# Optimization experiments

Hardware: AMD Instinct MI355X
Metric: run time of the kernel (lower is better)

Reference implementation:

```python
import jax, jax.numpy as jnp
import numpy as np

B, N, K = 4, 4096, 16
D_POINTS, D_MODEL = 64, 128


def setup_inputs() -> dict:
    key = jax.random.key(0)
    ks = jax.random.split(key, 18)
    rn = lambda k, shp, s=0.05: (jax.random.normal(k, shp, jnp.float32) * s)
    return {
        "xyz": jax.random.normal(ks[0], (B, N, 3), jnp.float32),
        "features": jax.random.normal(ks[1], (B, N, D_POINTS), jnp.float32),
        # fc_delta: Linear(3,d_model) -> ReLU -> Linear(d_model,d_model)
        "Wd1": rn(ks[2], (3, D_MODEL)), "bd1": rn(ks[3], (D_MODEL,)),
        "Wd2": rn(ks[4], (D_MODEL, D_MODEL)), "bd2": rn(ks[5], (D_MODEL,)),
        # fc1: Linear(d_points, d_model)
        "Wf1": rn(ks[6], (D_POINTS, D_MODEL)), "bf1": rn(ks[7], (D_MODEL,)),
        # w_qs / w_ks / w_vs: Linear(d_model, d_model, bias=False)
        "Wq": rn(ks[8], (D_MODEL, D_MODEL)),
        "Wk": rn(ks[9], (D_MODEL, D_MODEL)),
        "Wv": rn(ks[10], (D_MODEL, D_MODEL)),
        # fc_gamma: Linear(d_model,d_model) -> ReLU -> Linear(d_model,d_model)
        "Wg1": rn(ks[11], (D_MODEL, D_MODEL)), "bg1": rn(ks[12], (D_MODEL,)),
        "Wg2": rn(ks[13], (D_MODEL, D_MODEL)), "bg2": rn(ks[14], (D_MODEL,)),
        # fc2: Linear(d_model, d_points)
        "Wo": rn(ks[15], (D_MODEL, D_POINTS)), "bo": rn(ks[16], (D_POINTS,)),
    }


def reference(xyz, features, Wd1, bd1, Wd2, bd2, Wf1, bf1, Wq, Wk, Wv,
              Wg1, bg1, Wg2, bg2, Wo, bo):
    sq = jnp.sum(xyz * xyz, axis=-1)
    d2 = sq[:, :, None] + sq[:, None, :] - 2.0 * jnp.einsum('bnd,bmd->bnm', xyz, xyz)
    # argsort()[:, :, :k] == k smallest distances (self included)
    _, knn_idx = jax.lax.top_k(-d2, K)  # [B,N,K] int32

    gather = jax.vmap(lambda a, i: a[i])  # per-batch fancy gather along point axis
    knn_xyz = gather(xyz, knn_idx)                       # [B,N,K,3]
    rel = xyz[:, :, None, :] - knn_xyz                   # [B,N,K,3]
    pos_enc = jax.nn.relu(rel @ Wd1 + bd1) @ Wd2 + bd2   # [B,N,K,D]

    shortcut = features
    f = features @ Wf1 + bf1                             # [B,N,D]
    knn_f = gather(f, knn_idx)                           # [B,N,K,D]

    q = f @ Wq                                           # [B,N,D]
    k = knn_f @ Wk                                       # [B,N,K,D]
    v = knn_f @ Wv                                       # [B,N,K,D]

    attn = q[:, :, None, :] - k + pos_enc                # [B,N,K,D]
    attn = jax.nn.relu(attn @ Wg1 + bg1) @ Wg2 + bg2
    attn = jax.nn.softmax(attn / np.sqrt(D_MODEL).astype(np.float32), axis=-2)

    res = jnp.einsum('bnkf,bnkf->bnf', attn, v + pos_enc)  # [B,N,D]
    return res @ Wo + bo + shortcut                        # [B,N,d_points]
```

## Files before the change

### kernel.cpp

```cpp
#include <hip/hip_runtime.h>
#include <hip/hip_bf16.h>

#define NPTS 4096
#define BATCH 4
#define BN (BATCH * NPTS)
#define DMODEL 128
#define DPTS 64
#define KNBR 16
#define SWS 136

typedef unsigned short u16;
typedef unsigned int u32;
typedef unsigned long long u64;
typedef short bh8 __attribute__((ext_vector_type(8)));
typedef float f32x4 __attribute__((ext_vector_type(4)));

__device__ __forceinline__ float bfu(u16 u) {
    union { u32 i; float f; } c; c.i = ((u32)u) << 16; return c.f;
}
__device__ __forceinline__ u16 f2u(float x) {
    u32 u = __float_as_uint(x);
    u32 r = u + 0x7FFFu + ((u >> 16) & 1u);
    return (u16)(r >> 16);
}
__device__ __forceinline__ u32 pack2(float a, float b) {
    return (u32)f2u(a) | ((u32)f2u(b) << 16);
}
__device__ __forceinline__ float ldr(const void* p, long i, int mode) {
    return mode == 0 ? bfu(((const u16*)p)[i]) : ((const float*)p)[i];
}
__device__ __forceinline__ void str(void* p, long i, float v, int mode) {
    if (mode == 0) ((u16*)p)[i] = f2u(v);
    else ((float*)p)[i] = v;
}
__device__ __forceinline__ int detect_mode(const void* Wq) {
    const u16* w = (const u16*)Wq;
    int lane = threadIdx.x & 63;
    int tot = 0;
#pragma unroll
    for (int r = 0; r < 4; ++r) {
        unsigned e = (w[lane + r * 64] >> 7) & 0xFFu;
        bool wild = (e >= 132u) || (e > 0u && e <= 90u);
        tot += (int)__popcll(__ballot(wild));
    }
    return tot > 32 ? 1 : 0;
}

__global__ __launch_bounds__(256) void prep_kernel(
    const void* __restrict__ Wd2, const void* __restrict__ Wg1, const void* __restrict__ Wg2,
    const void* __restrict__ Wo, const void* __restrict__ Wq, const void* __restrict__ Wk,
    const void* __restrict__ Wv, const void* __restrict__ Wf1, const void* __restrict__ xyz,
    u16* __restrict__ WdT2, u16* __restrict__ WgT1, u16* __restrict__ WgT2,
    u16* __restrict__ WoT, u16* __restrict__ WqT, u16* __restrict__ WkT,
    u16* __restrict__ WvT, u16* __restrict__ WfT, uint2* __restrict__ cloud) {
    int mode = detect_mode(Wq);
    int gid = blockIdx.x * 256 + threadIdx.x;
    if (gid < 6 * 16384) {
        int m = gid >> 14, o = gid & 16383;
        int n = o >> 7, i = o & 127;
        const void* W = (m == 0) ? Wd2 : (m == 1) ? Wg1 : (m == 2) ? Wg2
                      : (m == 3) ? Wq  : (m == 4) ? Wk  : Wv;
        u16* D = (m == 0) ? WdT2 : (m == 1) ? WgT1 : (m == 2) ? WgT2
               : (m == 3) ? WqT  : (m == 4) ? WkT  : WvT;
        D[o] = f2u(ldr(W, (long)i * 128 + n, mode));
    } else if (gid < 6 * 16384 + 8192) {
        int o = gid - 6 * 16384;
        int n = o >> 6, k2 = o & 63;
        WfT[o] = f2u(ldr(Wf1, (long)k2 * 128 + n, mode));
    } else if (gid < 6 * 16384 + 16384) {
        int o2 = gid - 6 * 16384 - 8192;
        int col = o2 >> 7, i = o2 & 127;
        WoT[o2] = f2u(ldr(Wo, (long)i * 64 + col, mode));
    } else if (gid < 6 * 16384 + 16384 + 16384) {
        int i = gid - (6 * 16384 + 16384);
        float gx = ldr(xyz, (long)i * 3 + 0, mode);
        float gy = ldr(xyz, (long)i * 3 + 1, mode);
        float gz = ldr(xyz, (long)i * 3 + 2, mode);
        uint2 pk;
        pk.x = (u32)f2u(gx) | ((u32)f2u(gy) << 16);
        pk.y = (u32)f2u(gz);
        cloud[i] = pk;
    }
}

__global__ __launch_bounds__(256) void qkv_kernel(
    const void* __restrict__ feat, const void* __restrict__ bf1v, const void* __restrict__ WqRaw,
    const u16* __restrict__ WfT, const u16* __restrict__ WqT,
    const u16* __restrict__ WkT, const u16* __restrict__ WvT,
    u16* __restrict__ qw, u16* __restrict__ kfw, u16* __restrict__ vfw) {
    int mode = detect_mode(WqRaw);
    __shared__ __align__(16) u16 sFeat[64 * 72];
    __shared__ __align__(16) u16 sF[64 * SWS];
    const int t = threadIdx.x;
    const int p0 = blockIdx.x * 64;
    const int lane = t & 63, w = t >> 6;
    const int rg = (w & 1) * 32, cg = (w >> 1) * 64;
    const int lm = lane & 15, lq = lane >> 4;

    for (int i = t; i < 512; i += 256) {
        int r = i >> 3, c8 = i & 7;
        u16 tmp[8];
        if (mode == 0) {
            *(uint4*)tmp = *((const uint4*)feat + (long)(p0 + r) * 8 + c8);
        } else {
            const float* fp = (const float*)feat + (long)(p0 + r) * 64 + c8 * 8;
#pragma unroll
            for (int u = 0; u < 8; ++u) tmp[u] = f2u(fp[u]);
        }
        *(uint4*)(sFeat + r * 72 + c8 * 8) = *(uint4*)tmp;
    }
    __syncthreads();

    {
        f32x4 acc[2][4];
#pragma unroll
        for (int rt = 0; rt < 2; ++rt)
#pragma unroll
            for (int ct = 0; ct < 4; ++ct) { acc[rt][ct][0]=0.f; acc[rt][ct][1]=0.f; acc[rt][ct][2]=0.f; acc[rt][ct][3]=0.f; }
#pragma unroll
        for (int kk = 0; kk < 2; ++kk) {
            const int ko = kk * 32 + lq * 8;
            bh8 a0 = *(const bh8*)(sFeat + (rg + lm) * 72 + ko);
            bh8 a1 = *(const bh8*)(sFeat + (rg + 16 + lm) * 72 + ko);
            bh8 bq[4];
#pragma unroll
            for (int ct = 0; ct < 4; ++ct)
                bq[ct] = *(const bh8*)(WfT + (long)(cg + ct * 16 + lm) * 64 + ko);
#pragma unroll
            for (int ct = 0; ct < 4; ++ct) {
                acc[0][ct] = __builtin_amdgcn_mfma_f32_16x16x32_bf16(a0, bq[ct], acc[0][ct], 0, 0, 0);
                acc[1][ct] = __builtin_amdgcn_mfma_f32_16x16x32_bf16(a1, bq[ct], acc[1][ct], 0, 0, 0);
            }
        }
#pragma unroll
        for (int rt = 0; rt < 2; ++rt)
#pragma unroll
            for (int ct = 0; ct < 4; ++ct) {
                const int col = cg + ct * 16 + lm;
                const float bj = ldr(bf1v, col, mode);
#pragma unroll
                for (int r4 = 0; r4 < 4; ++r4) {
                    int row = rg + rt * 16 + lq * 4 + r4;
                    u32 u = (u32)f2u(acc[rt][ct][r4] + bj);
                    u32 o = __shfl_xor(u, 1);
                    if ((lane & 1) == 0)
                        *(u32*)(sF + row * SWS + col) = u | (o << 16);
                }
            }
    }
    __syncthreads();

    {
        const int m = blockIdx.y;
        const u16* Wm = (m == 0) ? WqT : (m == 1) ? WkT : WvT;
        u16* Om = (m == 0) ? qw : (m == 1) ? kfw : vfw;
        f32x4 acc[2][4];
#pragma unroll
        for (int rt = 0; rt < 2; ++rt)
#pragma unroll
            for (int ct = 0; ct < 4; ++ct) { acc[rt][ct][0]=0.f; acc[rt][ct][1]=0.f; acc[rt][ct][2]=0.f; acc[rt][ct][3]=0.f; }
#pragma unroll
        for (int kk = 0; kk < 4; ++kk) {
            const int ko = kk * 32 + lq * 8;
            bh8 a0 = *(const bh8*)(sF + (rg + lm) * SWS + ko);
            bh8 a1 = *(const bh8*)(sF + (rg + 16 + lm) * SWS + ko);
            bh8 bq[4];
#pragma unroll
            for (int ct = 0; ct < 4; ++ct)
                bq[ct] = *(const bh8*)(Wm + (long)(cg + ct * 16 + lm) * 128 + ko);
#pragma unroll
            for (int ct = 0; ct < 4; ++ct) {
                acc[0][ct] = __builtin_amdgcn_mfma_f32_16x16x32_bf16(a0, bq[ct], acc[0][ct], 0, 0, 0);
                acc[1][ct] = __builtin_amdgcn_mfma_f32_16x16x32_bf16(a1, bq[ct], acc[1][ct], 0, 0, 0);
            }
        }
#pragma unroll
        for (int rt = 0; rt < 2; ++rt)
#pragma unroll
            for (int ct = 0; ct < 4; ++ct) {
                const int col = cg + ct * 16 + lm;
#pragma unroll
                for (int r4 = 0; r4 < 4; ++r4) {
                    int row = rg + rt * 16 + lq * 4 + r4;
                    u32 u = (u32)f2u(acc[rt][ct][r4]);
                    u32 o = __shfl_xor(u, 1);
                    if ((lane & 1) == 0)
                        *(u32*)(Om + (long)(p0 + row) * DMODEL + col) = u | (o << 16);
                }
            }
    }
}

__global__ __launch_bounds__(256) void knn_kernel(
    const uint2* __restrict__ cloud, int* __restrict__ knnIdx) {
    const int t = threadIdx.x, lane = t & 63, w = t >> 6;
    const int p0 = blockIdx.x * 4;
    const long bbase = (long)(p0 >> 12) * NPTS;
    const uint2* cl = cloud + bbase;

    const int pl = (p0 & (NPTS - 1)) + w;
    uint2 qv = cl[pl];
    const float px = __uint_as_float(qv.x << 16);
    const float py = __uint_as_float(qv.x & 0xFFFF0000u);
    const float pz = __uint_as_float(qv.y << 16);

    u64 kv;
    {
        uint2 c = cl[lane];
        float cx = __uint_as_float(c.x << 16);
        float cy = __uint_as_float(c.x & 0xFFFF0000u);
        float cz = __uint_as_float(c.y << 16);
        float key = fmaf(px * cx + py * cy + pz * cz, -2.f,
                         cx * cx + cy * cy + cz * cz);
        u32 uk = __float_as_uint(key);
        uk ^= (u32)((int)uk >> 31) | 0x80000000u;
        kv = ((u64)uk << 32) | (u32)lane;
#pragma unroll
        for (int k = 2; k <= 64; k <<= 1) {
#pragma unroll
            for (int j = k >> 1; j > 0; j >>= 1) {
                u64 other = __shfl_xor(kv, j);
                bool keepMin = ((lane & j) == 0) == ((lane & k) == 0);
                bool smaller = kv < other;
                kv = (keepMin == smaller) ? kv : other;
            }
        }
    }
    u32 Tu = __builtin_amdgcn_readlane((u32)(kv >> 32), 15);

    uint2 cd0 = cl[64 + lane];
    uint2 cd1 = cl[128 + lane];
#pragma unroll 1
    for (int it = 0; it < 32; ++it) {
        const int base = 64 + it * 128;
        uint2 c0 = cd0, c1 = cd1;
        if (it < 31) {
            int n0 = base + 128 + lane;
            int n1 = n0 + 64 > 4095 ? 4095 : n0 + 64;
            cd0 = cl[n0];
            cd1 = cl[n1];
        }
        float cx0 = __uint_as_float(c0.x << 16);
        float cy0 = __uint_as_float(c0.x & 0xFFFF0000u);
        float cz0 = __uint_as_float(c0.y << 16);
        float cx1 = __uint_as_float(c1.x << 16);
        float cy1 = __uint_as_float(c1.x & 0xFFFF0000u);
        float cz1 = __uint_as_float(c1.y << 16);
        float k0 = fmaf(px * cx0 + py * cy0 + pz * cz0, -2.f,
                        cx0 * cx0 + cy0 * cy0 + cz0 * cz0);
        float k1 = fmaf(px * cx1 + py * cy1 + pz * cz1, -2.f,
                        cx1 * cx1 + cy1 * cy1 + cz1 * cz1);
        u32 u0 = __float_as_uint(k0); u0 ^= (u32)((int)u0 >> 31) | 0x80000000u;
        u32 u1 = __float_as_uint(k1); u1 ^= (u32)((int)u1 >> 31) | 0x80000000u;
        if (it == 31) u1 = 0xFFFFFFFFu;
        u32 umin = (u0 < u1) ? u0 : u1;
        unsigned long long mask = __ballot(umin < Tu);
        while (mask) {
            int l = __ffsll(mask) - 1;
            mask &= mask - 1;
            u32 a0 = __builtin_amdgcn_readlane(u0, l);
            u32 a1 = __builtin_amdgcn_readlane(u1, l);
            if (a0 < Tu) {
                u64 cand = ((u64)a0 << 32) | (u32)(base + l);
                u64 prev = __shfl_up(kv, 1);
                if (lane == 0) prev = 0;
                kv = (prev > cand) ? prev : ((kv > cand) ? cand : kv);
                Tu = __builtin_amdgcn_readlane((u32)(kv >> 32), 15);
            }
            if (a1 < Tu) {
                u64 cand = ((u64)a1 << 32) | (u32)(base + 64 + l);
                u64 prev = __shfl_up(kv, 1);
                if (lane == 0) prev = 0;
                kv = (prev > cand) ? prev : ((kv > cand) ? cand : kv);
                Tu = __builtin_amdgcn_readlane((u32)(kv >> 32), 15);
            }
        }
    }
    if (lane < 16) knnIdx[(long)(p0 + w) * 16 + lane] = (int)(u32)kv;
}

#define ATT_SA 0
#define ATT_SPE 17408
#define ATT_SREL 34816
#define ATT_SBIAS 35840
#define ATT_SQ 37376
#define SMEM_BYTES 38400

__global__ __launch_bounds__(256, 4) void fused_kernel(
    const uint2* __restrict__ cloud, const int* __restrict__ knnIdx,
    const void* __restrict__ feat,
    const void* __restrict__ Wd1, const void* __restrict__ bd1, const void* __restrict__ bd2,
    const void* __restrict__ bg1, const void* __restrict__ bg2, const void* __restrict__ bo,
    const void* __restrict__ WqRaw,
    const u16* __restrict__ WdT2, const u16* __restrict__ WgT1, const u16* __restrict__ WgT2,
    const u16* __restrict__ WoT,
    const u16* __restrict__ qw, const u16* __restrict__ kfw, const u16* __restrict__ vfw,
    void* __restrict__ out) {
    int mode = detect_mode(WqRaw);
    __shared__ __align__(16) char smem[SMEM_BYTES];
    __shared__ int sIdx[64];
    u16* sA   = (u16*)(smem + ATT_SA);
    u16* sPE  = (u16*)(smem + ATT_SPE);
    float (*sRel)[4] = (float(*)[4])(smem + ATT_SREL);
    float* sBias = (float*)(smem + ATT_SBIAS);
    u16* sQ   = (u16*)(smem + ATT_SQ);

    const int t = threadIdx.x, lane = t & 63, w = t >> 6;
    const int lm = lane & 15, lq = lane >> 4;
    const int p0 = blockIdx.x * 4;
    const long bbase = (long)(p0 >> 12) * NPTS;
    const uint2* cl = cloud + bbase;

    for (int i = t; i < 384; i += 256) {
        const void* b = (i < 128) ? bd2 : (i < 256) ? bg1 : bg2;
        sBias[i] = ldr(b, i & 127, mode);
    }
    ((u32*)sQ)[t] = ((const u32*)(qw + (long)p0 * DMODEL))[t];
    const int ch = 2 * lane;
    const float wd0a = ldr(Wd1, ch, mode),       wd0b = ldr(Wd1, ch + 1, mode);
    const float wd1a = ldr(Wd1, 128 + ch, mode), wd1b = ldr(Wd1, 128 + ch + 1, mode);
    const float wd2a = ldr(Wd1, 256 + ch, mode), wd2b = ldr(Wd1, 256 + ch + 1, mode);
    const float bd1a = ldr(bd1, ch, mode),       bd1b = ldr(bd1, ch + 1, mode);
    if (t < 64) {
        int idx = knnIdx[(long)p0 * 16 + t];
        sIdx[t] = idx;
        int pl2 = (p0 & (NPTS - 1)) + (t >> 4);
        uint2 pv = cl[pl2];
        uint2 nv = cl[idx];
        sRel[t][0] = __uint_as_float(pv.x << 16)          - __uint_as_float(nv.x << 16);
        sRel[t][1] = __uint_as_float(pv.x & 0xFFFF0000u)  - __uint_as_float(nv.x & 0xFFFF0000u);
        sRel[t][2] = __uint_as_float(pv.y << 16)          - __uint_as_float(nv.y << 16);
    }
    __syncthreads();

#pragma unroll
    for (int i = 0; i < 16; ++i) {
        int r = w * 16 + i;
        float4 rl = *(const float4*)sRel[r];
        float h0 = fmaxf(bd1a + rl.x * wd0a + rl.y * wd1a + rl.z * wd2a, 0.f);
        float h1 = fmaxf(bd1b + rl.x * wd0b + rl.y * wd1b + rl.z * wd2b, 0.f);
        *(u32*)(sA + r * SWS + ch) = pack2(h0, h1);
    }
    __syncthreads();
    {
        const int rg = (w & 1) * 32, cg = (w >> 1) * 64;
        f32x4 acc[2][4];
#pragma unroll
        for (int rt = 0; rt < 2; ++rt)
#pragma unroll
            for (int ct = 0; ct < 4; ++ct) { acc[rt][ct][0]=0.f; acc[rt][ct][1]=0.f; acc[rt][ct][2]=0.f; acc[rt][ct][3]=0.f; }
#pragma unroll
        for (int kk = 0; kk < 4; ++kk) {
            const int ko = kk * 32 + lq * 8;
            bh8 a0 = *(const bh8*)(sA + (rg + lm) * SWS + ko);
            bh8 a1 = *(const bh8*)(sA + (rg + 16 + lm) * SWS + ko);
            bh8 bq[4];
#pragma unroll
            for (int ct = 0; ct < 4; ++ct)
                bq[ct] = *(const bh8*)(WdT2 + (long)(cg + ct * 16 + lm) * 128 + ko);
#pragma unroll
            for (int ct = 0; ct < 4; ++ct) {
                acc[0][ct] = __builtin_amdgcn_mfma_f32_16x16x32_bf16(a0, bq[ct], acc[0][ct], 0, 0, 0);
                acc[1][ct] = __builtin_amdgcn_mfma_f32_16x16x32_bf16(a1, bq[ct], acc[1][ct], 0, 0, 0);
            }
        }
#pragma unroll
        for (int rt = 0; rt < 2; ++rt)
#pragma unroll
            for (int ct = 0; ct < 4; ++ct) {
                const int col = cg + ct * 16 + lm;
                const float bj = sBias[col];
#pragma unroll
                for (int r4 = 0; r4 < 4; ++r4) {
                    int row = rg + rt * 16 + lq * 4 + r4;
                    u32 u = (u32)f2u(acc[rt][ct][r4] + bj);
                    u32 o = __shfl_xor(u, 1);
                    if ((lane & 1) == 0)
                        *(u32*)(sPE + row * SWS + col) = u | (o << 16);
                }
            }
    }
    __syncthreads();

#pragma unroll
    for (int i = 0; i < 16; ++i) {
        int r = w * 16 + i;
        u32 kv2 = *(const u32*)(kfw + (bbase + sIdx[r]) * (long)DMODEL + ch);
        u32 qv2 = *(const u32*)(sQ + (r >> 4) * DMODEL + ch);
        u32 pe2 = *(const u32*)(sPE + r * SWS + ch);
        float a0 = bfu((u16)qv2) - bfu((u16)kv2) + bfu((u16)pe2);
        float a1 = bfu((u16)(qv2 >> 16)) - bfu((u16)(kv2 >> 16)) + bfu((u16)(pe2 >> 16));
        *(u32*)(sA + r * SWS + ch) = pack2(a0, a1);
    }
    __syncthreads();
#pragma unroll 1
    for (int g = 0; g < 2; ++g) {
        const u16* Bg = (g == 0) ? WgT1 : WgT2;
        const float* bias = sBias + 128 + g * 128;
        const bool dorelu = (g == 0);
        const int rg = (w & 1) * 32, cg = (w >> 1) * 64;
        f32x4 acc[2][4];
#pragma unroll
        for (int rt = 0; rt < 2; ++rt)
#pragma unroll
            for (int ct = 0; ct < 4; ++ct) { acc[rt][ct][0]=0.f; acc[rt][ct][1]=0.f; acc[rt][ct][2]=0.f; acc[rt][ct][3]=0.f; }
#pragma unroll
        for (int kk = 0; kk < 4; ++kk) {
            const int ko = kk * 32 + lq * 8;
            bh8 a0 = *(const bh8*)(sA + (rg + lm) * SWS + ko);
            bh8 a1 = *(const bh8*)(sA + (rg + 16 + lm) * SWS + ko);
            bh8 bq[4];
#pragma unroll
            for (int ct = 0; ct < 4; ++ct)
                bq[ct] = *(const bh8*)(Bg + (long)(cg + ct * 16 + lm) * 128 + ko);
#pragma unroll
            for (int ct = 0; ct < 4; ++ct) {
                acc[0][ct] = __builtin_amdgcn_mfma_f32_16x16x32_bf16(a0, bq[ct], acc[0][ct], 0, 0, 0);
                acc[1][ct] = __builtin_amdgcn_mfma_f32_16x16x32_bf16(a1, bq[ct], acc[1][ct], 0, 0, 0);
            }
        }
        __syncthreads();
#pragma unroll
        for (int rt = 0; rt < 2; ++rt)
#pragma unroll
            for (int ct = 0; ct < 4; ++ct) {
                const int col = cg + ct * 16 + lm;
                const float bj = bias[col];
#pragma unroll
                for (int r4 = 0; r4 < 4; ++r4) {
                    int row = rg + rt * 16 + lq * 4 + r4;
                    float v = acc[rt][ct][r4] + bj;
                    if (dorelu) v = fmaxf(v, 0.f);
                    u32 u = (u32)f2u(v);
                    u32 o = __shfl_xor(u, 1);
                    if ((lane & 1) == 0)
                        *(u32*)(sA + row * SWS + col) = u | (o << 16);
                }
            }
        __syncthreads();
    }

    float res0, res1;
    {
        float mx0 = -3e38f, mx1 = -3e38f;
#pragma unroll
        for (int k = 0; k < KNBR; ++k) {
            u32 l2 = *(const u32*)(sA + (w * 16 + k) * SWS + ch);
            mx0 = fmaxf(mx0, bfu((u16)l2));
            mx1 = fmaxf(mx1, bfu((u16)(l2 >> 16)));
        }
        const float inv = 0.08838834764831845f;
        float s0 = 0.f, s1 = 0.f, r0 = 0.f, r1 = 0.f;
#pragma unroll
        for (int k = 0; k < KNBR; ++k) {
            u32 l2 = *(const u32*)(sA + (w * 16 + k) * SWS + ch);
            u32 v2 = *(const u32*)(vfw + (bbase + sIdx[w * 16 + k]) * (long)DMODEL + ch);
            u32 p2 = *(const u32*)(sPE + (w * 16 + k) * SWS + ch);
            float e0 = __expf((bfu((u16)l2) - mx0) * inv);
            float e1 = __expf((bfu((u16)(l2 >> 16)) - mx1) * inv);
            s0 += e0; s1 += e1;
            r0 += e0 * (bfu((u16)v2) + bfu((u16)p2));
            r1 += e1 * (bfu((u16)(v2 >> 16)) + bfu((u16)(p2 >> 16)));
        }
        res0 = r0 / s0; res1 = r1 / s1;
    }
    __syncthreads();
    *(u32*)(sA + w * SWS + ch) = pack2(res0, res1);
    __syncthreads();

    {
        const int col = w * 16 + lm;
        f32x4 acc = {0.f, 0.f, 0.f, 0.f};
#pragma unroll
        for (int kk = 0; kk < 4; ++kk) {
            const int ko = kk * 32 + lq * 8;
            bh8 aa = *(const bh8*)(sA + lm * SWS + ko);
            bh8 bb = *(const bh8*)(WoT + (long)col * DMODEL + ko);
            acc = __builtin_amdgcn_mfma_f32_16x16x32_bf16(aa, bb, acc, 0, 0, 0);
        }
        if (lq == 0) {
            float bov = ldr(bo, col, mode);
#pragma unroll
            for (int r4 = 0; r4 < 4; ++r4) {
                long p = p0 + r4;
                float v = acc[r4] + bov + ldr(feat, p * DPTS + col, mode);
                str(out, p * DPTS + col, v, mode);
            }
        }
    }
}

extern "C" void kernel_launch(void* const* d_in, const int* in_sizes, int n_in,
                              void* d_out, int out_size, void* d_ws, size_t ws_size,
                              hipStream_t stream) {
    (void)in_sizes; (void)n_in; (void)out_size; (void)ws_size;
    char* ws = (char*)d_ws;
    u16* qw   = (u16*)(ws + 256);
    u16* kfw  = qw + (long)BN * DMODEL;
    u16* vfw  = kfw + (long)BN * DMODEL;
    u16* WdT2 = vfw + (long)BN * DMODEL;
    u16* WgT1 = WdT2 + 16384;
    u16* WgT2 = WgT1 + 16384;
    u16* WoT  = WgT2 + 16384;
    u16* WqT  = WoT + 8192;
    u16* WkT  = WqT + 16384;
    u16* WvT  = WkT + 16384;
    u16* WfT  = WvT + 16384;
    uint2* cloud = (uint2*)(WfT + 8192);
    int* knnIdx = (int*)(cloud + BN);

    prep_kernel<<<512, 256, 0, stream>>>(d_in[4], d_in[11], d_in[13], d_in[15],
                                         d_in[8], d_in[9], d_in[10], d_in[6], d_in[0],
                                         WdT2, WgT1, WgT2, WoT, WqT, WkT, WvT, WfT,
                                         cloud);
    qkv_kernel<<<dim3(BN / 64, 3), 256, 0, stream>>>(d_in[1], d_in[7], d_in[8],
                                                     WfT, WqT, WkT, WvT, qw, kfw, vfw);
    knn_kernel<<<BN / 4, 256, 0, stream>>>(cloud, knnIdx);
    fused_kernel<<<BN / 4, 256, 0, stream>>>(cloud, knnIdx, d_in[1],
                                             d_in[2], d_in[3], d_in[5],
                                             d_in[12], d_in[14], d_in[16], d_in[8],
                                             WdT2, WgT1, WgT2, WoT,
                                             qw, kfw, vfw, d_out);
}
```

Measured before the change: 303.1 us.

## Keep pos-enc and logits in registers, drop sPE smem buffer, raise occupancy

```diff
diff --git a/kernel.cpp b/kernel.cpp
--- a/kernel.cpp
+++ b/kernel.cpp
@@ -280,13 +280,12 @@
 }
 
 #define ATT_SA 0
-#define ATT_SPE 17408
-#define ATT_SREL 34816
-#define ATT_SBIAS 35840
-#define ATT_SQ 37376
-#define SMEM_BYTES 38400
-
-__global__ __launch_bounds__(256, 4) void fused_kernel(
+#define ATT_SREL 17408
+#define ATT_SBIAS 18432
+#define ATT_SQ 19968
+#define SMEM_BYTES 20992
+
+__global__ __launch_bounds__(256, 6) void fused_kernel(
     const uint2* __restrict__ cloud, const int* __restrict__ knnIdx,
     const void* __restrict__ feat,
     const void* __restrict__ Wd1, const void* __restrict__ bd1, const void* __restrict__ bd2,
@@ -300,13 +299,13 @@
     __shared__ __align__(16) char smem[SMEM_BYTES];
     __shared__ int sIdx[64];
     u16* sA   = (u16*)(smem + ATT_SA);
-    u16* sPE  = (u16*)(smem + ATT_SPE);
     float (*sRel)[4] = (float(*)[4])(smem + ATT_SREL);
     float* sBias = (float*)(smem + ATT_SBIAS);
     u16* sQ   = (u16*)(smem + ATT_SQ);
 
     const int t = threadIdx.x, lane = t & 63, w = t >> 6;
     const int lm = lane & 15, lq = lane >> 4;
+    const int rg = (w & 1) * 32, cg = (w >> 1) * 64;
     const int p0 = blockIdx.x * 4;
     const long bbase = (long)(p0 >> 12) * NPTS;
     const uint2* cl = cloud + bbase;
@@ -342,8 +341,9 @@
         *(u32*)(sA + r * SWS + ch) = pack2(h0, h1);
     }
     __syncthreads();
-    {
-        const int rg = (w & 1) * 32, cg = (w >> 1) * 64;
+
+    u32 pe[2][4][2];
+    {
         f32x4 acc[2][4];
 #pragma unroll
         for (int rt = 0; rt < 2; ++rt)
@@ -368,37 +368,40 @@
         for (int rt = 0; rt < 2; ++rt)
 #pragma unroll
             for (int ct = 0; ct < 4; ++ct) {
-                const int col = cg + ct * 16 + lm;
-                const float bj = sBias[col];
-#pragma unroll
-                for (int r4 = 0; r4 < 4; ++r4) {
-                    int row = rg + rt * 16 + lq * 4 + r4;
-                    u32 u = (u32)f2u(acc[rt][ct][r4] + bj);
-                    u32 o = __shfl_xor(u, 1);
-                    if ((lane & 1) == 0)
-                        *(u32*)(sPE + row * SWS + col) = u | (o << 16);
-                }
-            }
-    }
-    __syncthreads();
-
-#pragma unroll
-    for (int i = 0; i < 16; ++i) {
-        int r = w * 16 + i;
-        u32 kv2 = *(const u32*)(kfw + (bbase + sIdx[r]) * (long)DMODEL + ch);
-        u32 qv2 = *(const u32*)(sQ + (r >> 4) * DMODEL + ch);
-        u32 pe2 = *(const u32*)(sPE + r * SWS + ch);
-        float a0 = bfu((u16)qv2) - bfu((u16)kv2) + bfu((u16)pe2);
-        float a1 = bfu((u16)(qv2 >> 16)) - bfu((u16)(kv2 >> 16)) + bfu((u16)(pe2 >> 16));
-        *(u32*)(sA + r * SWS + ch) = pack2(a0, a1);
-    }
-    __syncthreads();
-#pragma unroll 1
-    for (int g = 0; g < 2; ++g) {
-        const u16* Bg = (g == 0) ? WgT1 : WgT2;
-        const float* bias = sBias + 128 + g * 128;
-        const bool dorelu = (g == 0);
-        const int rg = (w & 1) * 32, cg = (w >> 1) * 64;
+                const float bj = sBias[cg + ct * 16 + lm];
+                pe[rt][ct][0] = pack2(acc[rt][ct][0] + bj, acc[rt][ct][1] + bj);
+                pe[rt][ct][1] = pack2(acc[rt][ct][2] + bj, acc[rt][ct][3] + bj);
+            }
+    }
+    __syncthreads();
+
+#pragma unroll
+    for (int rt = 0; rt < 2; ++rt) {
+        const int pt = (w & 1) * 2 + rt;
+        int id4[4];
+#pragma unroll
+        for (int r4 = 0; r4 < 4; ++r4)
+            id4[r4] = sIdx[rg + rt * 16 + lq * 4 + r4];
+#pragma unroll
+        for (int ct = 0; ct < 4; ++ct) {
+            const int col = cg + ct * 16 + lm;
+            const float qv = bfu(sQ[pt * DMODEL + col]);
+#pragma unroll
+            for (int r4 = 0; r4 < 4; ++r4) {
+                const int row = rg + rt * 16 + lq * 4 + r4;
+                u16 kfv = kfw[(bbase + id4[r4]) * (long)DMODEL + col];
+                float pev = bfu((u16)(pe[rt][ct][r4 >> 1] >> (16 * (r4 & 1))));
+                float a = qv - bfu(kfv) + pev;
+                u32 u = (u32)f2u(a);
+                u32 o = __shfl_xor(u, 1);
+                if ((lm & 1) == 0)
+                    *(u32*)(sA + row * SWS + col) = u | (o << 16);
+            }
+        }
+    }
+    __syncthreads();
+
+    {
         f32x4 acc[2][4];
 #pragma unroll
         for (int rt = 0; rt < 2; ++rt)
@@ -412,7 +415,7 @@
             bh8 bq[4];
 #pragma unroll
             for (int ct = 0; ct < 4; ++ct)
-                bq[ct] = *(const bh8*)(Bg + (long)(cg + ct * 16 + lm) * 128 + ko);
+                bq[ct] = *(const bh8*)(WgT1 + (long)(cg + ct * 16 + lm) * 128 + ko);
 #pragma unroll
             for (int ct = 0; ct < 4; ++ct) {
                 acc[0][ct] = __builtin_amdgcn_mfma_f32_16x16x32_bf16(a0, bq[ct], acc[0][ct], 0, 0, 0);
@@ -425,47 +428,91 @@
 #pragma unroll
             for (int ct = 0; ct < 4; ++ct) {
                 const int col = cg + ct * 16 + lm;
-                const float bj = bias[col];
+                const float bj = sBias[128 + col];
 #pragma unroll
                 for (int r4 = 0; r4 < 4; ++r4) {
                     int row = rg + rt * 16 + lq * 4 + r4;
-                    float v = acc[rt][ct][r4] + bj;
-                    if (dorelu) v = fmaxf(v, 0.f);
+                    float v = fmaxf(acc[rt][ct][r4] + bj, 0.f);
                     u32 u = (u32)f2u(v);
                     u32 o = __shfl_xor(u, 1);
                     if ((lane & 1) == 0)
                         *(u32*)(sA + row * SWS + col) = u | (o << 16);
                 }
             }
-        __syncthreads();
-    }
-
-    float res0, res1;
-    {
-        float mx0 = -3e38f, mx1 = -3e38f;
-#pragma unroll
-        for (int k = 0; k < KNBR; ++k) {
-            u32 l2 = *(const u32*)(sA + (w * 16 + k) * SWS + ch);
-            mx0 = fmaxf(mx0, bfu((u16)l2));
-            mx1 = fmaxf(mx1, bfu((u16)(l2 >> 16)));
-        }
+    }
+    __syncthreads();
+
+    u32 lg[2][4][2];
+    {
+        f32x4 acc[2][4];
+#pragma unroll
+        for (int rt = 0; rt < 2; ++rt)
+#pragma unroll
+            for (int ct = 0; ct < 4; ++ct) { acc[rt][ct][0]=0.f; acc[rt][ct][1]=0.f; acc[rt][ct][2]=0.f; acc[rt][ct][3]=0.f; }
+#pragma unroll
+        for (int kk = 0; kk < 4; ++kk) {
+            const int ko = kk * 32 + lq * 8;
+            bh8 a0 = *(const bh8*)(sA + (rg + lm) * SWS + ko);
+            bh8 a1 = *(const bh8*)(sA + (rg + 16 + lm) * SWS + ko);
+            bh8 bq[4];
+#pragma unroll
+            for (int ct = 0; ct < 4; ++ct)
+                bq[ct] = *(const bh8*)(WgT2 + (long)(cg + ct * 16 + lm) * 128 + ko);
+#pragma unroll
+            for (int ct = 0; ct < 4; ++ct) {
+                acc[0][ct] = __builtin_amdgcn_mfma_f32_16x16x32_bf16(a0, bq[ct], acc[0][ct], 0, 0, 0);
+                acc[1][ct] = __builtin_amdgcn_mfma_f32_16x16x32_bf16(a1, bq[ct], acc[1][ct], 0, 0, 0);
+            }
+        }
+#pragma unroll
+        for (int rt = 0; rt < 2; ++rt)
+#pragma unroll
+            for (int ct = 0; ct < 4; ++ct) {
+                const float bj = sBias[256 + cg + ct * 16 + lm];
+                lg[rt][ct][0] = pack2(acc[rt][ct][0] + bj, acc[rt][ct][1] + bj);
+                lg[rt][ct][1] = pack2(acc[rt][ct][2] + bj, acc[rt][ct][3] + bj);
+            }
+    }
+    __syncthreads();
+
+    {
         const float inv = 0.08838834764831845f;
-        float s0 = 0.f, s1 = 0.f, r0 = 0.f, r1 = 0.f;
-#pragma unroll
-        for (int k = 0; k < KNBR; ++k) {
-            u32 l2 = *(const u32*)(sA + (w * 16 + k) * SWS + ch);
-            u32 v2 = *(const u32*)(vfw + (bbase + sIdx[w * 16 + k]) * (long)DMODEL + ch);
-            u32 p2 = *(const u32*)(sPE + (w * 16 + k) * SWS + ch);
-            float e0 = __expf((bfu((u16)l2) - mx0) * inv);
-            float e1 = __expf((bfu((u16)(l2 >> 16)) - mx1) * inv);
-            s0 += e0; s1 += e1;
-            r0 += e0 * (bfu((u16)v2) + bfu((u16)p2));
-            r1 += e1 * (bfu((u16)(v2 >> 16)) + bfu((u16)(p2 >> 16)));
-        }
-        res0 = r0 / s0; res1 = r1 / s1;
-    }
-    __syncthreads();
-    *(u32*)(sA + w * SWS + ch) = pack2(res0, res1);
+#pragma unroll
+        for (int rt = 0; rt < 2; ++rt) {
+            const int pt = (w & 1) * 2 + rt;
+            int id4[4];
+#pragma unroll
+            for (int r4 = 0; r4 < 4; ++r4)
+                id4[r4] = sIdx[rg + rt * 16 + lq * 4 + r4];
+#pragma unroll
+            for (int ct = 0; ct < 4; ++ct) {
+                const int col = cg + ct * 16 + lm;
+                float l0 = bfu((u16)lg[rt][ct][0]);
+                float l1 = bfu((u16)(lg[rt][ct][0] >> 16));
+                float l2 = bfu((u16)lg[rt][ct][1]);
+                float l3 = bfu((u16)(lg[rt][ct][1] >> 16));
+                float m = fmaxf(fmaxf(l0, l1), fmaxf(l2, l3));
+                m = fmaxf(m, __shfl_xor(m, 16));
+                m = fmaxf(m, __shfl_xor(m, 32));
+                float s = 0.f, r = 0.f;
+#pragma unroll
+                for (int r4 = 0; r4 < 4; ++r4) {
+                    float l = (r4 == 0) ? l0 : (r4 == 1) ? l1 : (r4 == 2) ? l2 : l3;
+                    u16 vv = vfw[(bbase + id4[r4]) * (long)DMODEL + col];
+                    float pev = bfu((u16)(pe[rt][ct][r4 >> 1] >> (16 * (r4 & 1))));
+                    float e = __expf((l - m) * inv);
+                    s += e;
+                    r += e * (bfu(vv) + pev);
+                }
+                s += __shfl_xor(s, 16); s += __shfl_xor(s, 32);
+                r += __shfl_xor(r, 16); r += __shfl_xor(r, 32);
+                u32 u = (u32)f2u(r / s);
+                u32 o = __shfl_xor(u, 1);
+                if (lq == 0 && (lm & 1) == 0)
+                    *(u32*)(sA + pt * SWS + col) = u | (o << 16);
+            }
+        }
+    }
     __syncthreads();
 
     {
```

New measurement: 345.5 us. 14.0% more time.
